# Kernel tuning notes

Measured on AMD Instinct MI355X. Metric: run time of the kernel, lower is better.

The kernel has to match this reference:

```python
import jax, jax.numpy as jnp
import numpy as np

B, S, E, H = 4, 512, 1024, 16
DH = E // H
SCALE = 1.0 / float(np.sqrt(DH))


def setup_inputs() -> dict:
    key = jax.random.key(0)
    ks = jax.random.split(key, 6)
    x_val = jax.random.normal(ks[0], (B, S, E), dtype=jnp.float32)
    eps = 0.1 * jax.random.uniform(ks[1], (B, S, E), dtype=jnp.float32)
    x_lb = x_val - eps
    x_ub = x_val + eps
    s = 1.0 / float(np.sqrt(E))
    in_proj_w = jax.random.uniform(ks[2], (E, 3 * E), jnp.float32, -s, s)
    in_proj_b = jax.random.uniform(ks[3], (3 * E,), jnp.float32, -s, s)
    out_proj_w = jax.random.uniform(ks[4], (E, E), jnp.float32, -s, s)
    out_proj_b = jax.random.uniform(ks[5], (E,), jnp.float32, -s, s)
    return dict(x_val=x_val, x_lb=x_lb, x_ub=x_ub,
                in_proj_w=in_proj_w, in_proj_b=in_proj_b,
                out_proj_w=out_proj_w, out_proj_b=out_proj_b)


def _pos(x):
    return jnp.maximum(x, 0.0)


def _neg(x):
    return jnp.minimum(x, 0.0)


def ibp_linear(v, l, u, W, b):
    # interval input x point weight: lb' = lb@W+ + ub@W-,  ub' = ub@W+ + lb@W-
    Wp, Wn = _pos(W), _neg(W)
    return v @ W + b, l @ Wp + u @ Wn + b, u @ Wp + l @ Wn + b


def ibp_matmul(av, al, au, bv, bl, bu):
    # interval x interval matmul with the 4-way clamp decomposition (as in ibp.matmul)
    val = av @ bv
    lb = (_pos(al) @ _pos(bl) + _pos(au) @ _neg(bl)
          + _neg(al) @ _pos(bu) + _neg(au) @ _neg(bu))
    ub = (_pos(au) @ _pos(bu) + _pos(al) @ _neg(bu)
          + _neg(au) @ _pos(bl) + _neg(al) @ _neg(bl))
    return val, lb, ub


def ibp_softmax(v, l, u):
    # p_i lower bound: exp(lb_i) / (exp(lb_i) + sum_{j!=i} exp(ub_j)); symmetric for upper
    pv = jax.nn.softmax(v, axis=-1)
    m = jnp.max(u, axis=-1, keepdims=True)
    e_l = jnp.exp(l - m)
    e_u = jnp.exp(u - m)
    S_l = jnp.sum(e_l, axis=-1, keepdims=True)
    S_u = jnp.sum(e_u, axis=-1, keepdims=True)
    pl = e_l / (S_u - e_u + e_l)
    pu = e_u / (S_l - e_l + e_u)
    return pv, jnp.clip(pl, 0.0, 1.0), jnp.clip(pu, 0.0, 1.0)


def _heads(x):  # [B,S,E] -> [B,H,S,DH]
    return x.reshape(B, S, H, DH).transpose(0, 2, 1, 3)


def _merge(x):  # [B,H,S,DH] -> [B,S,E]
    return x.transpose(0, 2, 1, 3).reshape(B, S, E)


def reference(x_val, x_lb, x_ub, in_proj_w, in_proj_b, out_proj_w, out_proj_b):
    qkv_v, qkv_l, qkv_u = ibp_linear(x_val, x_lb, x_ub, in_proj_w, in_proj_b)

    def split(t):
        q, k, v = jnp.split(t, 3, axis=-1)
        return _heads(q), _heads(k), _heads(v)

    (qv, kv, vv) = split(qkv_v)
    (ql, kl, vl) = split(qkv_l)
    (qu, ku, vu) = split(qkv_u)
    # positive scalar scale preserves bound ordering
    qv, ql, qu = qv * SCALE, ql * SCALE, qu * SCALE
    kT = lambda x: x.transpose(0, 1, 3, 2)
    sv, sl, su = ibp_matmul(qv, ql, qu, kT(kv), kT(kl), kT(ku))  # [B,H,S,S]
    pv, pl, pu = ibp_softmax(sv, sl, su)
    ov, ol, ou = ibp_matmul(pv, pl, pu, vv, vl, vu)  # [B,H,S,DH]
    ov, ol, ou = _merge(ov), _merge(ol), _merge(ou)
    yv, yl, yu = ibp_linear(ov, ol, ou, out_proj_w, out_proj_b)
    return jnp.stack([yv, yl, yu])  # [3,B,S,E]
```

## Files before the change

### kernel.cpp

```cpp
#include <hip/hip_runtime.h>
#include <math.h>

#define SEQ    512
#define EMB    1024
#define NHEAD  16
#define DHEAD  64
#define NBAT   4
#define QSCALE 0.125f
#define KS     72
#define VS     40

typedef __attribute__((ext_vector_type(8))) short bf16x8;
typedef __attribute__((ext_vector_type(4))) float f32x4;

#define MFMA16(a, b, c) __builtin_amdgcn_mfma_f32_16x16x32_bf16(a, b, c, 0, 0, 0)

__device__ __forceinline__ unsigned short f2b(float x) {
  union { float f; unsigned int u; } a; a.f = x;
  unsigned int u = a.u;
  unsigned int r = (u + 0x7fffu + ((u >> 16) & 1u)) >> 16;
  return (unsigned short)r;
}
__device__ __forceinline__ unsigned short f2b_fast(float x) {
  union { float f; unsigned int u; } a; a.f = x;
  return (unsigned short)((a.u + 0x8000u) >> 16);
}
__device__ __forceinline__ float b2f(unsigned short x) {
  union { unsigned int u; float f; } a; a.u = ((unsigned int)x) << 16; return a.f;
}

__device__ __forceinline__ void async16(const unsigned short* g, unsigned short* lds) {
  __builtin_amdgcn_global_load_lds(
      (const __attribute__((address_space(1))) unsigned int*)g,
      (__attribute__((address_space(3))) unsigned int*)lds, 16, 0, 0);
}

__device__ __forceinline__ void clamp_pn8(bf16x8 x, bf16x8* p, bf16x8* n) {
  const unsigned int* xu = (const unsigned int*)&x;
  unsigned int* pp = (unsigned int*)p;
  unsigned int* nn = (unsigned int*)n;
#pragma unroll
  for (int e = 0; e < 4; e++) {
    const unsigned int s = xu[e] & 0x80008000u;
    const unsigned int mask = s | (s - (s >> 15));
    nn[e] = xu[e] & mask;
    pp[e] = xu[e] & ~mask;
  }
}

__device__ __forceinline__ float wave16_sum(float x) {
#pragma unroll
  for (int m = 1; m <= 8; m <<= 1) x += __shfl_xor(x, m);
  return x;
}

__global__ __launch_bounds__(256)
void convert_stack(const float* __restrict__ v, const float* __restrict__ l,
                   const float* __restrict__ u,
                   unsigned short* __restrict__ outV,
                   unsigned short* __restrict__ outC,
                   unsigned short* __restrict__ outR, int total4)
{
  int i = blockIdx.x * 256 + threadIdx.x;
  if (i >= total4) return;
  float4 v4 = ((const float4*)v)[i];
  float4 l4 = ((const float4*)l)[i];
  float4 u4 = ((const float4*)u)[i];
  float lv[4] = {l4.x, l4.y, l4.z, l4.w};
  float uv[4] = {u4.x, u4.y, u4.z, u4.w};
  float vv[4] = {v4.x, v4.y, v4.z, v4.w};
  ushort4 ov, oc, orr;
  unsigned short* pv = (unsigned short*)&ov;
  unsigned short* pc = (unsigned short*)&oc;
  unsigned short* pr = (unsigned short*)&orr;
#pragma unroll
  for (int e = 0; e < 4; e++) {
    pv[e] = f2b(vv[e]);
    pc[e] = f2b(0.5f * (lv[e] + uv[e]));
    pr[e] = f2b(0.5f * (uv[e] - lv[e]));
  }
  ((ushort4*)outV)[i] = ov;
  ((ushort4*)outC)[i] = oc;
  ((ushort4*)outR)[i] = orr;
}

__global__ __launch_bounds__(256)
void wt_convert(const float* __restrict__ W,
                unsigned short* __restrict__ Wt,
                unsigned short* __restrict__ Wa, int K, int N)
{
  __shared__ float tile[32][33];
  const int n0 = blockIdx.x * 32, k0 = blockIdx.y * 32;
  const int tx = threadIdx.x, ty = threadIdx.y;
#pragma unroll
  for (int r = 0; r < 32; r += 8)
    tile[ty + r][tx] = W[(size_t)(k0 + ty + r) * N + n0 + tx];
  __syncthreads();
#pragma unroll
  for (int r = 0; r < 32; r += 8) {
    const float w = tile[tx][ty + r];
    const size_t o = (size_t)(n0 + ty + r) * K + k0 + tx;
    Wt[o] = f2b(w);
    Wa[o] = f2b(fabsf(w));
  }
}

template<int BN>
__global__ __launch_bounds__(256, 2)
void gemm_ibp3(const unsigned short* __restrict__ Av,
               const unsigned short* __restrict__ Ac,
               const unsigned short* __restrict__ Ar,
               const unsigned short* __restrict__ Bt,
               const unsigned short* __restrict__ Ba,
               int K, const float* __restrict__ bias,
               float* __restrict__ oV, float* __restrict__ oL, float* __restrict__ oU,
               unsigned short* __restrict__ hV, unsigned short* __restrict__ hL,
               unsigned short* __restrict__ hU,
               unsigned short* __restrict__ vtV, unsigned short* __restrict__ vtL,
               unsigned short* __restrict__ vtU, int N)
{
  constexpr int NF = BN / 32;
  __shared__ __attribute__((aligned(16))) unsigned short Avs[2][64 * 32];
  __shared__ __attribute__((aligned(16))) unsigned short Acs[2][64 * 32];
  __shared__ __attribute__((aligned(16))) unsigned short Ars[2][64 * 32];
  __shared__ __attribute__((aligned(16))) unsigned short Bts[2][BN * 32];
  __shared__ __attribute__((aligned(16))) unsigned short Bas[2][BN * 32];

  const int t = threadIdx.x, lane = t & 63, w = t >> 6;
  const int m0 = blockIdx.y * 64, n0 = blockIdx.x * BN;
  const int wm = w & 1, wn = w >> 1;
  const int quad = lane >> 4, r16 = lane & 15;
  const int srow = lane >> 2, sseg = lane & 3;

  f32x4 av[2][NF], ac[2][NF], ar[2][NF];
#pragma unroll
  for (int i = 0; i < 2; i++)
#pragma unroll
    for (int j = 0; j < NF; j++) {
      av[i][j] = (f32x4){0.f, 0.f, 0.f, 0.f};
      ac[i][j] = (f32x4){0.f, 0.f, 0.f, 0.f};
      ar[i][j] = (f32x4){0.f, 0.f, 0.f, 0.f};
    }

  const int iters = K >> 5;
  auto stage = [&](int it, int buf) {
    const int k0 = it * 32;
    const size_t ga = (size_t)(m0 + 16 * w + srow) * K + k0 + sseg * 8;
    async16(Av + ga, &Avs[buf][16 * w * 32]);
    async16(Ac + ga, &Acs[buf][16 * w * 32]);
    async16(Ar + ga, &Ars[buf][16 * w * 32]);
#pragma unroll
    for (int r = 0; r < BN / 64; r++) {
      const int brow = (BN / 4) * w + 16 * r;
      const size_t gb = (size_t)(n0 + brow + srow) * K + k0 + sseg * 8;
      async16(Bt + gb, &Bts[buf][brow * 32]);
      async16(Ba + gb, &Bas[buf][brow * 32]);
    }
  };

  stage(0, 0);
  for (int it = 0; it < iters; ++it) {
    const int cur = it & 1;
    __syncthreads();
    if (it + 1 < iters) stage(it + 1, cur ^ 1);
    bf16x8 fv[2], fc[2], fr[2], gt[NF], gb[NF];
#pragma unroll
    for (int i = 0; i < 2; i++) {
      const int off = (wm * 32 + i * 16 + r16) * 32 + quad * 8;
      fv[i] = *(const bf16x8*)(&Avs[cur][off]);
      fc[i] = *(const bf16x8*)(&Acs[cur][off]);
      fr[i] = *(const bf16x8*)(&Ars[cur][off]);
    }
#pragma unroll
    for (int j = 0; j < NF; j++) {
      const int off = (wn * (BN / 2) + j * 16 + r16) * 32 + quad * 8;
      gt[j] = *(const bf16x8*)(&Bts[cur][off]);
      gb[j] = *(const bf16x8*)(&Bas[cur][off]);
    }
#pragma unroll
    for (int i = 0; i < 2; i++)
#pragma unroll
      for (int j = 0; j < NF; j++) {
        av[i][j] = MFMA16(fv[i], gt[j], av[i][j]);
        ac[i][j] = MFMA16(fc[i], gt[j], ac[i][j]);
        ar[i][j] = MFMA16(fr[i], gb[j], ar[i][j]);
      }
  }

#pragma unroll
  for (int i = 0; i < 2; i++) {
    const int mbase = m0 + wm * 32 + i * 16 + quad * 4;
#pragma unroll
    for (int j = 0; j < NF; j++) {
      const int n = n0 + wn * (BN / 2) + j * 16 + r16;
      const float bv = bias[n];
      float vv[4], lv[4], uv[4];
#pragma unroll
      for (int rI = 0; rI < 4; rI++) {
        const float c = ac[i][j][rI], r = ar[i][j][rI];
        vv[rI] = av[i][j][rI] + bv;
        lv[rI] = c - r + bv;
        uv[rI] = c + r + bv;
      }
      if (hV) {
#pragma unroll
        for (int rI = 0; rI < 4; rI++) {
          hV[(size_t)(mbase + rI) * N + n] = f2b(vv[rI]);
          hL[(size_t)(mbase + rI) * N + n] = f2b(lv[rI]);
          hU[(size_t)(mbase + rI) * N + n] = f2b(uv[rI]);
        }
      } else {
#pragma unroll
        for (int rI = 0; rI < 4; rI++) {
          oV[(size_t)(mbase + rI) * N + n] = vv[rI];
          oL[(size_t)(mbase + rI) * N + n] = lv[rI];
          oU[(size_t)(mbase + rI) * N + n] = uv[rI];
        }
      }
      if (vtV && n >= 2048) {
        const int hh = (n - 2048) >> 6, dd = (n - 2048) & 63;
        const int bb = mbase >> 9, ss = mbase & 511;
        ushort4 v4, l4, u4;
        unsigned short* vp = (unsigned short*)&v4;
        unsigned short* lp = (unsigned short*)&l4;
        unsigned short* up = (unsigned short*)&u4;
#pragma unroll
        for (int rI = 0; rI < 4; rI++) {
          vp[rI] = f2b(vv[rI]); lp[rI] = f2b(lv[rI]); up[rI] = f2b(uv[rI]);
        }
        const size_t vo = (size_t)((bb * 16 + hh) * 64 + dd) * 512 + ss;
        *(ushort4*)(vtV + vo) = v4;
        *(ushort4*)(vtL + vo) = l4;
        *(ushort4*)(vtU + vo) = u4;
      }
    }
  }
}

__device__ __forceinline__ void qk_tile(const unsigned short* K0,
                                        const unsigned short* K1,
                                        const unsigned short* K2,
                                        int cl, int quad,
                                        const bf16x8 qvf[2], const bf16x8 qlpf[2],
                                        const bf16x8 qlnf[2], const bf16x8 qupf[2],
                                        const bf16x8 qunf[2],
                                        f32x4* avp, f32x4* alp, f32x4* aup)
{
  f32x4 v = {0.f, 0.f, 0.f, 0.f}, l = v, u = v;
#pragma unroll
  for (int kh = 0; kh < 2; kh++) {
    const int off = cl * KS + kh * 32 + quad * 8;
    bf16x8 kv = *(const bf16x8*)(K0 + off);
    bf16x8 kl = *(const bf16x8*)(K1 + off);
    bf16x8 ku = *(const bf16x8*)(K2 + off);
    bf16x8 klp, kln, kup, kun;
    clamp_pn8(kl, &klp, &kln);
    clamp_pn8(ku, &kup, &kun);
    v = MFMA16(qvf[kh], kv, v);
    l = MFMA16(qlpf[kh], klp, l);
    l = MFMA16(qupf[kh], kln, l);
    l = MFMA16(qlnf[kh], kup, l);
    l = MFMA16(qunf[kh], kun, l);
    u = MFMA16(qupf[kh], kup, u);
    u = MFMA16(qlpf[kh], kun, u);
    u = MFMA16(qunf[kh], klp, u);
    u = MFMA16(qlnf[kh], kln, u);
  }
  *avp = v; *alp = l; *aup = u;
}

__global__ __launch_bounds__(256, 4)
void ibp_attn_mfma(const unsigned short* __restrict__ qkv_v,
                   const unsigned short* __restrict__ qkv_l,
                   const unsigned short* __restrict__ qkv_u,
                   const unsigned short* __restrict__ vt_v,
                   const unsigned short* __restrict__ vt_l,
                   const unsigned short* __restrict__ vt_u,
                   unsigned short* __restrict__ Ov,
                   unsigned short* __restrict__ Oc,
                   unsigned short* __restrict__ Or)
{
  __shared__ __attribute__((aligned(16))) unsigned short pool[6912 + 7680 + 3840];
  __shared__ float st[2][32][3];
  unsigned short* Ks = pool;
  unsigned short* Vs = pool + 6912;
  unsigned short* Ps = pool + 6912 + 7680;

  const int qblk = blockIdx.x, h = blockIdx.y, b = blockIdx.z;
  const int t = threadIdx.x, lane = t & 63, w = t >> 6;
  const int wm = w >> 1, wc = w & 1;
  const int quad = lane >> 4, r16 = lane & 15;
  const int mq = b * SEQ + qblk * 32;
  const int bh = b * NHEAD + h;

  bf16x8 qvf[2], qlpf[2], qlnf[2], qupf[2], qunf[2];
  {
    const size_t qrow = (size_t)(mq + wm * 16 + r16) * 3072 + h * 64;
#pragma unroll
    for (int kh = 0; kh < 2; kh++) {
      bf16x8 v8 = *(const bf16x8*)(qkv_v + qrow + kh * 32 + quad * 8);
      bf16x8 l8 = *(const bf16x8*)(qkv_l + qrow + kh * 32 + quad * 8);
      bf16x8 u8 = *(const bf16x8*)(qkv_u + qrow + kh * 32 + quad * 8);
      const unsigned short* vs = (const unsigned short*)&v8;
      const unsigned short* ls = (const unsigned short*)&l8;
      const unsigned short* us = (const unsigned short*)&u8;
      unsigned short* ov = (unsigned short*)&qvf[kh];
      unsigned short* lp = (unsigned short*)&qlpf[kh];
      unsigned short* ln = (unsigned short*)&qlnf[kh];
      unsigned short* up = (unsigned short*)&qupf[kh];
      unsigned short* un = (unsigned short*)&qunf[kh];
#pragma unroll
      for (int e = 0; e < 8; e++) {
        ov[e] = f2b(b2f(vs[e]) * QSCALE);
        const float lf = b2f(ls[e]) * QSCALE;
        const float uf = b2f(us[e]) * QSCALE;
        lp[e] = f2b(fmaxf(lf, 0.f)); ln[e] = f2b(fminf(lf, 0.f));
        up[e] = f2b(fmaxf(uf, 0.f)); un[e] = f2b(fminf(uf, 0.f));
      }
    }
  }

  const int cl = wc * 16 + r16;
  const int krow = t >> 3, kseg = t & 7;
  const int vrow = t >> 2, vseg = t & 3;
  const unsigned short* kplane[3] = {qkv_v, qkv_l, qkv_u};
  const unsigned short* vplane[3] = {vt_v, vt_l, vt_u};

  float Svp[4] = {0.f, 0.f, 0.f, 0.f};
  float Slp[4] = {0.f, 0.f, 0.f, 0.f};
  float Sup[4] = {0.f, 0.f, 0.f, 0.f};

#pragma unroll
  for (int pI = 0; pI < 3; pI++)
    *(uint4*)(Ks + pI * 2304 + krow * KS + kseg * 8) =
        *(const uint4*)(kplane[pI] + (size_t)(b * SEQ + krow) * 3072 + 1024 + h * 64 + kseg * 8);
  __syncthreads();

  for (int ct = 0; ct < 16; ct++) {
    const unsigned short* cur = (ct & 1) ? Vs : Ks;
    if (ct < 15) {
      unsigned short* nxt = (ct & 1) ? Ks : Vs;
      const int c0n = (ct + 1) * 32;
#pragma unroll
      for (int pI = 0; pI < 3; pI++)
        *(uint4*)(nxt + pI * 2304 + krow * KS + kseg * 8) =
            *(const uint4*)(kplane[pI] + (size_t)(b * SEQ + c0n + krow) * 3072 + 1024 + h * 64 + kseg * 8);
    }
    f32x4 av, al, au;
    qk_tile(cur, cur + 2304, cur + 4608, cl, quad,
            qvf, qlpf, qlnf, qupf, qunf, &av, &al, &au);
#pragma unroll
    for (int r = 0; r < 4; r++) {
      Svp[r] += __expf(av[r]);
      Slp[r] += __expf(al[r]);
      Sup[r] += __expf(au[r]);
    }
    __syncthreads();
  }

#pragma unroll
  for (int r = 0; r < 4; r++) {
    Svp[r] = wave16_sum(Svp[r]);
    Slp[r] = wave16_sum(Slp[r]);
    Sup[r] = wave16_sum(Sup[r]);
  }
  if (r16 == 0) {
#pragma unroll
    for (int r = 0; r < 4; r++) {
      st[wc][wm * 16 + quad * 4 + r][0] = Svp[r];
      st[wc][wm * 16 + quad * 4 + r][1] = Slp[r];
      st[wc][wm * 16 + quad * 4 + r][2] = Sup[r];
    }
  }
  __syncthreads();
  float rSv4[4], Sl4[4], Su4[4];
#pragma unroll
  for (int r = 0; r < 4; r++) {
    const int row = wm * 16 + quad * 4 + r;
    rSv4[r] = 1.f / (st[0][row][0] + st[1][row][0]);
    Sl4[r]  = st[0][row][1] + st[1][row][1];
    Su4[r]  = st[0][row][2] + st[1][row][2];
  }

  f32x4 oa[3][2];
#pragma unroll
  for (int bo = 0; bo < 3; bo++)
#pragma unroll
    for (int ds = 0; ds < 2; ds++) oa[bo][ds] = (f32x4){0.f, 0.f, 0.f, 0.f};

  for (int ct = 0; ct < 16; ct++) {
    const int c0 = ct * 32;
    __syncthreads();
#pragma unroll
    for (int pI = 0; pI < 3; pI++) {
      *(uint4*)(Ks + pI * 2304 + krow * KS + kseg * 8) =
          *(const uint4*)(kplane[pI] + (size_t)(b * SEQ + c0 + krow) * 3072 + 1024 + h * 64 + kseg * 8);
      *(uint4*)(Vs + pI * 2560 + vrow * VS + vseg * 8) =
          *(const uint4*)(vplane[pI] + (size_t)(bh * 64 + vrow) * 512 + c0 + vseg * 8);
    }
    __syncthreads();

    f32x4 av, al, au;
    qk_tile(Ks, Ks + 2304, Ks + 4608, cl, quad,
            qvf, qlpf, qlnf, qupf, qunf, &av, &al, &au);
#pragma unroll
    for (int r = 0; r < 4; r++) {
      const float ev = __expf(av[r]);
      const float el = __expf(al[r]);
      const float eu = __expf(au[r]);
      float pl = el * __builtin_amdgcn_rcpf(Su4[r] - eu + el);
      float pu = eu * __builtin_amdgcn_rcpf(Sl4[r] - el + eu);
      pl = fminf(fmaxf(pl, 0.f), 1.f);
      pu = fminf(fmaxf(pu, 0.f), 1.f);
      const float pev = __shfl_xor(ev, 1);
      const float ppl = __shfl_xor(pl, 1);
      const float ppu = __shfl_xor(pu, 1);
      if (!(r16 & 1)) {
        const unsigned int wv = (unsigned int)f2b_fast(ev) | ((unsigned int)f2b_fast(pev) << 16);
        const unsigned int wl = (unsigned int)f2b_fast(pl) | ((unsigned int)f2b_fast(ppl) << 16);
        const unsigned int wu = (unsigned int)f2b_fast(pu) | ((unsigned int)f2b_fast(ppu) << 16);
        const int prow = (wm * 16 + quad * 4 + r) * VS + cl;
        *(unsigned int*)(Ps + prow)        = wv;
        *(unsigned int*)(Ps + 1280 + prow) = wl;
        *(unsigned int*)(Ps + 2560 + prow) = wu;
      }
    }
    __syncthreads();

#pragma unroll
    for (int ds = 0; ds < 2; ds++) {
      const int dsub = wc * 2 + ds;
      const int voff = (dsub * 16 + r16) * VS + quad * 8;
      bf16x8 vv = *(const bf16x8*)(Vs + voff);
      bf16x8 vl = *(const bf16x8*)(Vs + 2560 + voff);
      bf16x8 vu = *(const bf16x8*)(Vs + 5120 + voff);
      bf16x8 vlp, vln, vup, vun;
      clamp_pn8(vl, &vlp, &vln);
      clamp_pn8(vu, &vup, &vun);
      const int arow = (wm * 16 + r16) * VS + quad * 8;
      bf16x8 pav = *(const bf16x8*)(Ps + arow);
      bf16x8 pal = *(const bf16x8*)(Ps + 1280 + arow);
      bf16x8 pau = *(const bf16x8*)(Ps + 2560 + arow);
      oa[0][ds] = MFMA16(pav, vv, oa[0][ds]);
      oa[1][ds] = MFMA16(pal, vlp, oa[1][ds]);
      oa[1][ds] = MFMA16(pau, vln, oa[1][ds]);
      oa[2][ds] = MFMA16(pau, vup, oa[2][ds]);
      oa[2][ds] = MFMA16(pal, vun, oa[2][ds]);
    }
  }

#pragma unroll
  for (int ds = 0; ds < 2; ds++) {
    const int dsub = wc * 2 + ds;
#pragma unroll
    for (int r = 0; r < 4; r++) {
      const size_t row = (size_t)(mq + wm * 16 + quad * 4 + r);
      const int col = h * 64 + dsub * 16 + r16;
      const float ovv = oa[0][ds][r] * rSv4[r];
      const float olv = oa[1][ds][r];
      const float ouv = oa[2][ds][r];
      Ov[row * 1024 + col] = f2b(ovv);
      Oc[row * 1024 + col] = f2b(0.5f * (olv + ouv));
      Or[row * 1024 + col] = f2b(0.5f * (ouv - olv));
    }
  }
}

extern "C" void kernel_launch(void* const* d_in, const int* in_sizes, int n_in,
                              void* d_out, int out_size, void* d_ws, size_t ws_size,
                              hipStream_t stream)
{
  const float* x_val = (const float*)d_in[0];
  const float* x_lb  = (const float*)d_in[1];
  const float* x_ub  = (const float*)d_in[2];
  const float* Wi    = (const float*)d_in[3];
  const float* bi    = (const float*)d_in[4];
  const float* Wo    = (const float*)d_in[5];
  const float* bo    = (const float*)d_in[6];
  float* out = (float*)d_out;

  char* p = (char*)d_ws;
  unsigned short* Xv  = (unsigned short*)p; p += (size_t)2048 * 1024 * 2;
  unsigned short* Xc  = (unsigned short*)p; p += (size_t)2048 * 1024 * 2;
  unsigned short* Xr  = (unsigned short*)p; p += (size_t)2048 * 1024 * 2;
  unsigned short* Wit = (unsigned short*)p; p += (size_t)3072 * 1024 * 2;
  unsigned short* Wia = (unsigned short*)p; p += (size_t)3072 * 1024 * 2;
  unsigned short* Wot = (unsigned short*)p; p += (size_t)1024 * 1024 * 2;
  unsigned short* Woa = (unsigned short*)p; p += (size_t)1024 * 1024 * 2;
  unsigned short* qv  = (unsigned short*)p; p += (size_t)2048 * 3072 * 2;
  unsigned short* ql  = (unsigned short*)p; p += (size_t)2048 * 3072 * 2;
  unsigned short* qu  = (unsigned short*)p; p += (size_t)2048 * 3072 * 2;
  unsigned short* Vtv = (unsigned short*)p; p += (size_t)64 * 64 * 512 * 2;
  unsigned short* Vtl = (unsigned short*)p; p += (size_t)64 * 64 * 512 * 2;
  unsigned short* Vtu = (unsigned short*)p; p += (size_t)64 * 64 * 512 * 2;

  convert_stack<<<2048, 256, 0, stream>>>(x_val, x_lb, x_ub, Xv, Xc, Xr, 524288);
  wt_convert<<<dim3(96, 32), dim3(32, 8), 0, stream>>>(Wi, Wit, Wia, 1024, 3072);
  wt_convert<<<dim3(32, 32), dim3(32, 8), 0, stream>>>(Wo, Wot, Woa, 1024, 1024);

  gemm_ibp3<128><<<dim3(3072 / 128, 32), 256, 0, stream>>>(
      Xv, Xc, Xr, Wit, Wia, 1024, bi,
      nullptr, nullptr, nullptr, qv, ql, qu, Vtv, Vtl, Vtu, 3072);

  ibp_attn_mfma<<<dim3(SEQ / 32, NHEAD, NBAT), 256, 0, stream>>>(
      qv, ql, qu, Vtv, Vtl, Vtu, Xv, Xc, Xr);

  gemm_ibp3<64><<<dim3(1024 / 64, 32), 256, 0, stream>>>(
      Xv, Xc, Xr, Wot, Woa, 1024, bo,
      out, out + (size_t)2048 * 1024, out + (size_t)4096 * 1024,
      nullptr, nullptr, nullptr, nullptr, nullptr, nullptr, 1024);
}
```

Before: 313.9 us.

## Load GEMM A-operands directly from global into registers, shrink out-proj tile

The three A-operand tiles (value, center, radius) no longer go through LDS double-buffering. Each wave now loads its MFMA fragments straight from global memory before the barrier, and only the B weights stay staged in shared memory. The kernel gains a BM template parameter, and the output projection uses 32x64 tiles to launch more blocks. It also drops the min-blocks launch bound. This removes LDS traffic and capacity for A, which should raise occupancy, but it exposes uncoalesced global latency each iteration with no prefetch.

```diff
diff --git a/kernel.cpp b/kernel.cpp
--- a/kernel.cpp
+++ b/kernel.cpp
@@ -105,8 +105,8 @@
   }
 }
 
-template<int BN>
-__global__ __launch_bounds__(256, 2)
+template<int BM, int BN>
+__global__ __launch_bounds__(256)
 void gemm_ibp3(const unsigned short* __restrict__ Av,
                const unsigned short* __restrict__ Ac,
                const unsigned short* __restrict__ Ar,
@@ -119,24 +119,22 @@
                unsigned short* __restrict__ vtV, unsigned short* __restrict__ vtL,
                unsigned short* __restrict__ vtU, int N)
 {
-  constexpr int NF = BN / 32;
-  __shared__ __attribute__((aligned(16))) unsigned short Avs[2][64 * 32];
-  __shared__ __attribute__((aligned(16))) unsigned short Acs[2][64 * 32];
-  __shared__ __attribute__((aligned(16))) unsigned short Ars[2][64 * 32];
+  constexpr int MI = BM / 32;
+  constexpr int NJ = BN / 32;
   __shared__ __attribute__((aligned(16))) unsigned short Bts[2][BN * 32];
   __shared__ __attribute__((aligned(16))) unsigned short Bas[2][BN * 32];
 
   const int t = threadIdx.x, lane = t & 63, w = t >> 6;
-  const int m0 = blockIdx.y * 64, n0 = blockIdx.x * BN;
+  const int m0 = blockIdx.y * BM, n0 = blockIdx.x * BN;
   const int wm = w & 1, wn = w >> 1;
   const int quad = lane >> 4, r16 = lane & 15;
   const int srow = lane >> 2, sseg = lane & 3;
 
-  f32x4 av[2][NF], ac[2][NF], ar[2][NF];
-#pragma unroll
-  for (int i = 0; i < 2; i++)
-#pragma unroll
-    for (int j = 0; j < NF; j++) {
+  f32x4 av[MI][NJ], ac[MI][NJ], ar[MI][NJ];
+#pragma unroll
+  for (int i = 0; i < MI; i++)
+#pragma unroll
+    for (int j = 0; j < NJ; j++) {
       av[i][j] = (f32x4){0.f, 0.f, 0.f, 0.f};
       ac[i][j] = (f32x4){0.f, 0.f, 0.f, 0.f};
       ar[i][j] = (f32x4){0.f, 0.f, 0.f, 0.f};
@@ -145,10 +143,6 @@
   const int iters = K >> 5;
   auto stage = [&](int it, int buf) {
     const int k0 = it * 32;
-    const size_t ga = (size_t)(m0 + 16 * w + srow) * K + k0 + sseg * 8;
-    async16(Av + ga, &Avs[buf][16 * w * 32]);
-    async16(Ac + ga, &Acs[buf][16 * w * 32]);
-    async16(Ar + ga, &Ars[buf][16 * w * 32]);
 #pragma unroll
     for (int r = 0; r < BN / 64; r++) {
       const int brow = (BN / 4) * w + 16 * r;
@@ -161,37 +155,39 @@
   stage(0, 0);
   for (int it = 0; it < iters; ++it) {
     const int cur = it & 1;
+    const int k0 = it * 32;
+    bf16x8 fv[MI], fc[MI], fr[MI];
+#pragma unroll
+    for (int i = 0; i < MI; i++) {
+      const size_t ga = (size_t)(m0 + wm * (BM / 2) + i * 16 + r16) * K + k0 + quad * 8;
+      fv[i] = *(const bf16x8*)(Av + ga);
+      fc[i] = *(const bf16x8*)(Ac + ga);
+      fr[i] = *(const bf16x8*)(Ar + ga);
+    }
     __syncthreads();
     if (it + 1 < iters) stage(it + 1, cur ^ 1);
-    bf16x8 fv[2], fc[2], fr[2], gt[NF], gb[NF];
-#pragma unroll
-    for (int i = 0; i < 2; i++) {
-      const int off = (wm * 32 + i * 16 + r16) * 32 + quad * 8;
-      fv[i] = *(const bf16x8*)(&Avs[cur][off]);
-      fc[i] = *(const bf16x8*)(&Acs[cur][off]);
-      fr[i] = *(const bf16x8*)(&Ars[cur][off]);
-    }
-#pragma unroll
-    for (int j = 0; j < NF; j++) {
+    bf16x8 gt[NJ], gb_[NJ];
+#pragma unroll
+    for (int j = 0; j < NJ; j++) {
       const int off = (wn * (BN / 2) + j * 16 + r16) * 32 + quad * 8;
-      gt[j] = *(const bf16x8*)(&Bts[cur][off]);
-      gb[j] = *(const bf16x8*)(&Bas[cur][off]);
-    }
-#pragma unroll
-    for (int i = 0; i < 2; i++)
-#pragma unroll
-      for (int j = 0; j < NF; j++) {
+      gt[j]  = *(const bf16x8*)(&Bts[cur][off]);
+      gb_[j] = *(const bf16x8*)(&Bas[cur][off]);
+    }
+#pragma unroll
+    for (int i = 0; i < MI; i++)
+#pragma unroll
+      for (int j = 0; j < NJ; j++) {
         av[i][j] = MFMA16(fv[i], gt[j], av[i][j]);
         ac[i][j] = MFMA16(fc[i], gt[j], ac[i][j]);
-        ar[i][j] = MFMA16(fr[i], gb[j], ar[i][j]);
+        ar[i][j] = MFMA16(fr[i], gb_[j], ar[i][j]);
       }
   }
 
 #pragma unroll
-  for (int i = 0; i < 2; i++) {
-    const int mbase = m0 + wm * 32 + i * 16 + quad * 4;
-#pragma unroll
-    for (int j = 0; j < NF; j++) {
+  for (int i = 0; i < MI; i++) {
+    const int mbase = m0 + wm * (BM / 2) + i * 16 + quad * 4;
+#pragma unroll
+    for (int j = 0; j < NJ; j++) {
       const int n = n0 + wn * (BN / 2) + j * 16 + r16;
       const float bv = bias[n];
       float vv[4], lv[4], uv[4];
@@ -498,14 +494,14 @@
   wt_convert<<<dim3(96, 32), dim3(32, 8), 0, stream>>>(Wi, Wit, Wia, 1024, 3072);
   wt_convert<<<dim3(32, 32), dim3(32, 8), 0, stream>>>(Wo, Wot, Woa, 1024, 1024);
 
-  gemm_ibp3<128><<<dim3(3072 / 128, 32), 256, 0, stream>>>(
+  gemm_ibp3<64, 128><<<dim3(3072 / 128, 2048 / 64), 256, 0, stream>>>(
       Xv, Xc, Xr, Wit, Wia, 1024, bi,
       nullptr, nullptr, nullptr, qv, ql, qu, Vtv, Vtl, Vtu, 3072);
 
   ibp_attn_mfma<<<dim3(SEQ / 32, NHEAD, NBAT), 256, 0, stream>>>(
       qv, ql, qu, Vtv, Vtl, Vtu, Xv, Xc, Xr);
 
-  gemm_ibp3<64><<<dim3(1024 / 64, 32), 256, 0, stream>>>(
+  gemm_ibp3<32, 64><<<dim3(1024 / 64, 2048 / 32), 256, 0, stream>>>(
       Xv, Xc, Xr, Wot, Woa, 1024, bo,
       out, out + (size_t)2048 * 1024, out + (size_t)4096 * 1024,
       nullptr, nullptr, nullptr, nullptr, nullptr, nullptr, 1024);
```

Result: slower. 394.1 us (+25.5%).
